# Kernel tuning notes

Measured on AMD Instinct MI355X. Metric: run time of the kernel, lower is better.

## Reference

```python
import jax, jax.numpy as jnp
import numpy as np
from jax import lax

ANG_RES = 9
MINDISP = -4
MAXDISP = 4
DN = ('NCHW', 'OIHW', 'NCHW')


def _dilat_pad(d, ang):
    if d < 0:
        dilat = abs(d) * ang + 1
        pad = (ang * (ang - 1) * abs(d)) // 2
    elif d == 0:
        dilat = 1
        pad = 0
    else:
        dilat = abs(d) * ang - 1
        pad = (ang * (ang - 1) * abs(d)) // 2 - ang + 1
    return dilat, pad


def setup_inputs() -> dict:
    key = jax.random.key(0)
    k1, k2 = jax.random.split(key)
    x = jax.random.normal(k1, (4, 64, 432, 432), dtype=jnp.float32)  # [B, Cin, angRes*H, angRes*W]
    W = jax.random.normal(k2, (64, 64, 9, 9), dtype=jnp.float32) * 0.05  # [Cout, Cin, angRes, angRes]
    return {"x": x, "W": W}


def reference(x, W):
    costs = []
    for d in range(MINDISP, MAXDISP + 1):
        dilat, pad = _dilat_pad(d, ANG_RES)
        cost = lax.conv_general_dilated(
            x, W,
            window_strides=(ANG_RES, ANG_RES),
            padding=[(pad, pad), (pad, pad)],
            rhs_dilation=(dilat, dilat),
            dimension_numbers=DN,
        )  # [B, Cout, H, W]
        costs.append(cost)
    # stack along new disparity axis -> [B, Cout, D, H, W]
    return jnp.stack(costs, axis=2)
```

## Files before the change

kernel.cpp:

```cpp
#include <hip/hip_runtime.h>

#define ANG 9
#define OHW 48
#define IMG 432
#define CIN 64
#define COUT 64
#define ND 9
#define NB 4
#define NVIEW 81
#define NSPAT 2304
#define NTOT 9216

#define SLABW 81
#define SLABSZ (80 * SLABW)

using f32x4 = __attribute__((ext_vector_type(4))) float;
using s16x8 = __attribute__((ext_vector_type(8))) short;

__device__ __forceinline__ unsigned short f2bf(float f) {
    unsigned u = __float_as_uint(f);
    unsigned r = (u + 0x7FFFu + ((u >> 16) & 1u)) >> 16;
    return (unsigned short)r;
}

__global__ void k_wpack(const float* __restrict__ w, unsigned short* __restrict__ aw) {
    int idx = blockIdx.x * 256 + threadIdx.x;
    if (idx >= NVIEW * 128 * 64) return;
    int ci = idx & 63;
    int m  = (idx >> 6) & 127;
    int uv = idx >> 13;
    int u = uv / 9, v = uv % 9;
    int co = m & 63, var = m >> 6;
    int uu = var ? 8 - u : u;
    int vv = var ? 8 - v : v;
    aw[idx] = f2bf(w[((size_t)(co * 64 + ci) * 9 + uu) * 9 + vv]);
}

__global__ __launch_bounds__(512, 4)
void k_fused(const float* __restrict__ x,
             const unsigned short* __restrict__ aw,
             unsigned short* __restrict__ y) {
    __shared__ unsigned short lx[IMG * 64];
    const int h = blockIdx.x, u = blockIdx.y, b = blockIdx.z;
    const int t = threadIdx.x;
    const int ih = 9 * h + u;
    const int lane = t & 63, wave = t >> 6;
    const int lr = lane & 15;
    const int lh = lane >> 4;
    const int mh = wave >> 2;
    const int mf = wave & 3;

    const unsigned short* abase =
        aw + (((size_t)(u * 9) * 128) + mh * 64 + mf * 16 + lr) * 64 + lh * 8;
    s16x8 a0[9];
#pragma unroll
    for (int v = 0; v < 9; ++v)
        a0[v] = *reinterpret_cast<const s16x8*>(abase + (size_t)v * 128 * 64);

    {
        const int tx = t & 127, ty = t >> 7;
        if (tx < 108) {
            const float* base = x + (((size_t)b * 64) * IMG + ih) * IMG + 4 * tx;
#pragma unroll 4
            for (int k = 0; k < 16; ++k) {
                const int ci = ty * 16 + k;
                const float4 v4 = *reinterpret_cast<const float4*>(
                    base + (size_t)ci * (IMG * IMG));
                unsigned short us[4] = {f2bf(v4.x), f2bf(v4.y), f2bf(v4.z), f2bf(v4.w)};
#pragma unroll
                for (int jj = 0; jj < 4; ++jj) {
                    const int iw = 4 * tx + jj;
                    const int sc = ci ^ (((iw >> 2) & 7) << 3);
                    lx[iw * 64 + sc] = us[jj];
                }
            }
        }
    }
    __syncthreads();

    const int m    = mh * 64 + mf * 16 + lr;
    const int n0g  = b * NSPAT + h * 48;

    s16x8 a1n = *reinterpret_cast<const s16x8*>(abase + 32);
#pragma unroll
    for (int v = 0; v < 9; ++v) {
        const int uv = u * 9 + v;
        const s16x8 a1 = a1n;
        if (v < 8)
            a1n = *reinterpret_cast<const s16x8*>(abase + (size_t)(v + 1) * 128 * 64 + 32);
#pragma unroll
        for (int nt = 0; nt < 3; ++nt) {
            const int iw = 9 * (nt * 16 + lr) + v;
            const int g  = (iw >> 2) & 7;
            const s16x8 b0 = *reinterpret_cast<const s16x8*>(&lx[iw * 64 + ((lh ^ g) * 8)]);
            const s16x8 b1 = *reinterpret_cast<const s16x8*>(&lx[iw * 64 + (((4 + lh) ^ g) * 8)]);

            f32x4 acc = (f32x4){0.f, 0.f, 0.f, 0.f};
            acc = __builtin_amdgcn_mfma_f32_16x16x32_bf16(b0, a0[v], acc, 0, 0, 0);
            acc = __builtin_amdgcn_mfma_f32_16x16x32_bf16(b1, a1,    acc, 0, 0, 0);

            const unsigned long long pk =
                  (unsigned long long)f2bf(acc[0])
                | ((unsigned long long)f2bf(acc[1]) << 16)
                | ((unsigned long long)f2bf(acc[2]) << 32)
                | ((unsigned long long)f2bf(acc[3]) << 48);
            *reinterpret_cast<unsigned long long*>(
                &y[((size_t)uv * 128 + m) * NTOT + n0g + nt * 16 + 4 * lh]) = pk;
        }
    }
}

__global__ __launch_bounds__(576)
void k_gather4(const unsigned short* __restrict__ y, float* __restrict__ out) {
    __shared__ float lds[2 * SLABSZ];
    const int co = blockIdx.x, b = blockIdx.y;
    const int tid = threadIdx.x;

    for (int i = tid; i < 2 * SLABSZ; i += 576) lds[i] = 0.f;

    const int var  = tid / 288;
    const int e0   = (tid % 288) * 8;
    const int srow = e0 / 48, scol = e0 % 48;
    const int ldst = var * SLABSZ + (16 + srow) * SLABW + 16 + scol;
    const unsigned short* ybase =
        y + ((size_t)(var * 64 + co)) * NTOT + (size_t)b * NSPAT + e0;

    const int hh = tid / 12;
    const int w0 = (tid % 12) * 4;
    const int center = (16 + hh) * SLABW + 16 + w0;

    float acc[9][4];
#pragma unroll
    for (int dd = 0; dd < 9; ++dd)
#pragma unroll
        for (int i = 0; i < 4; ++i) acc[dd][i] = 0.f;

    uint4 pre0 = *reinterpret_cast<const uint4*>(ybase);
    uint4 pre1 = *reinterpret_cast<const uint4*>(ybase + (size_t)128 * NTOT);
    __syncthreads();

    for (int uv = 0; uv < NVIEW; ++uv) {
        float4 lo, hi;
        lo.x = __uint_as_float(pre0.x << 16);
        lo.y = __uint_as_float(pre0.x & 0xffff0000u);
        lo.z = __uint_as_float(pre0.y << 16);
        lo.w = __uint_as_float(pre0.y & 0xffff0000u);
        hi.x = __uint_as_float(pre0.z << 16);
        hi.y = __uint_as_float(pre0.z & 0xffff0000u);
        hi.z = __uint_as_float(pre0.w << 16);
        hi.w = __uint_as_float(pre0.w & 0xffff0000u);
        *reinterpret_cast<float4*>(&lds[ldst])     = lo;
        *reinterpret_cast<float4*>(&lds[ldst + 4]) = hi;

        pre0 = pre1;
        if (uv + 2 < NVIEW)
            pre1 = *reinterpret_cast<const uint4*>(ybase + (size_t)(uv + 2) * 128 * NTOT);

        __syncthreads();

        const int uq = uv / 9, vq = uv % 9;
        const int step = (uq - 4) * SLABW + (vq - 4);
        int base = center + 4 * step;
#pragma unroll
        for (int dd = 0; dd < 9; ++dd) {
            const float* p = &lds[base + (dd > 4 ? SLABSZ : 0)];
            acc[dd][0] += p[0];
            acc[dd][1] += p[1];
            acc[dd][2] += p[2];
            acc[dd][3] += p[3];
            base -= step;
        }
        __syncthreads();
    }

    const size_t ob = (size_t)(b * 64 + co) * 9 * NSPAT + tid * 4;
#pragma unroll
    for (int dd = 0; dd < 9; ++dd) {
        float4 o;
        o.x = acc[dd][0]; o.y = acc[dd][1]; o.z = acc[dd][2]; o.w = acc[dd][3];
        *reinterpret_cast<float4*>(&out[ob + (size_t)dd * NSPAT]) = o;
    }
}

__global__ __launch_bounds__(192)
void cost_volume_direct(const float* __restrict__ x,
                        const float* __restrict__ w,
                        float* __restrict__ out) {
    const int ow      = threadIdx.x;
    const int oh      = blockIdx.y * 4 + threadIdx.y;
    const int co_tile = blockIdx.x & 7;
    const int dd      = blockIdx.x >> 3;
    const int b       = blockIdx.z;
    const int d       = dd - 4;
    const int co0     = co_tile * 8;

    int dilat, pad;
    if (d < 0)       { dilat = (-d) * ANG + 1; pad = 36 * (-d); }
    else if (d == 0) { dilat = 1;              pad = 0; }
    else             { dilat = d * ANG - 1;    pad = 36 * d - (ANG - 1); }

    const int ih0 = oh * ANG - pad;
    const int iw0 = ow * ANG - pad;

    float acc[8];
#pragma unroll
    for (int i = 0; i < 8; ++i) acc[i] = 0.f;

    const float* xb = x + (size_t)b * CIN * IMG * IMG;
    for (int kh = 0; kh < ANG; ++kh) {
        const int ih = ih0 + kh * dilat;
        if ((unsigned)ih >= (unsigned)IMG) continue;
        const float* xrow_base = xb + (size_t)ih * IMG;
        const float* wrow      = w + kh * ANG;
        for (int ci = 0; ci < CIN; ++ci) {
            const float* xrow = xrow_base + (size_t)ci * (IMG * IMG);
            float xv[ANG];
#pragma unroll
            for (int kw = 0; kw < ANG; ++kw) {
                const int iw  = iw0 + kw * dilat;
                const bool ok = ((unsigned)iw < (unsigned)IMG);
                const float vv = xrow[ok ? iw : 0];
                xv[kw] = ok ? vv : 0.f;
            }
            const float* wc = wrow + ci * (ANG * ANG);
#pragma unroll
            for (int i = 0; i < 8; ++i) {
                const float* wi = wc + (size_t)(co0 + i) * (CIN * ANG * ANG);
#pragma unroll
                for (int kw = 0; kw < ANG; ++kw)
                    acc[i] = fmaf(xv[kw], wi[kw], acc[i]);
            }
        }
    }
#pragma unroll
    for (int i = 0; i < 8; ++i) {
        const size_t o = ((((size_t)b * COUT + (co0 + i)) * ND + dd) * OHW + oh) * OHW + ow;
        out[o] = acc[i];
    }
}

extern "C" void kernel_launch(void* const* d_in, const int* in_sizes, int n_in,
                              void* d_out, int out_size, void* d_ws, size_t ws_size,
                              hipStream_t stream) {
    const float* x   = (const float*)d_in[0];
    const float* w   = (const float*)d_in[1];
    float*       out = (float*)d_out;

    const size_t AW_BYTES = (size_t)NVIEW * 128 * 64 * 2;
    const size_t Y_BYTES  = (size_t)NVIEW * 128 * NTOT * 2;
    const size_t NEED     = AW_BYTES + Y_BYTES;

    if (ws_size >= NEED) {
        unsigned short* aw = (unsigned short*)d_ws;
        unsigned short* yb = (unsigned short*)((char*)d_ws + AW_BYTES);

        k_wpack  <<<dim3((NVIEW * 128 * 64 + 255) / 256), dim3(256), 0, stream>>>(w, aw);
        k_fused  <<<dim3(OHW, ANG, NB), dim3(512), 0, stream>>>(x, aw, yb);
        k_gather4<<<dim3(COUT, NB), dim3(576), 0, stream>>>(yb, out);
    } else {
        dim3 grid(8 * ND, OHW / 4, NB);
        dim3 block(OHW, 4, 1);
        cost_volume_direct<<<grid, block, 0, stream>>>(x, w, out);
    }
}
```

Measured before the change: 227.4 us.

## Process batch in two halves to shrink intermediate buffer for cache residency

After: 320.1 us. 40.8% more time.

```diff
diff --git a/kernel.cpp b/kernel.cpp
--- a/kernel.cpp
+++ b/kernel.cpp
@@ -9,7 +9,7 @@
 #define NB 4
 #define NVIEW 81
 #define NSPAT 2304
-#define NTOT 9216
+#define NTOTP 4608
 
 #define SLABW 81
 #define SLABSZ (80 * SLABW)
@@ -39,9 +39,10 @@
 __global__ __launch_bounds__(512, 4)
 void k_fused(const float* __restrict__ x,
              const unsigned short* __restrict__ aw,
-             unsigned short* __restrict__ y) {
+             unsigned short* __restrict__ y, int pair) {
     __shared__ unsigned short lx[IMG * 64];
-    const int h = blockIdx.x, u = blockIdx.y, b = blockIdx.z;
+    const int h = blockIdx.x, u = blockIdx.y, bl = blockIdx.z;
+    const int b = pair * 2 + bl;
     const int t = threadIdx.x;
     const int ih = 9 * h + u;
     const int lane = t & 63, wave = t >> 6;
@@ -78,8 +79,8 @@
     }
     __syncthreads();
 
-    const int m    = mh * 64 + mf * 16 + lr;
-    const int n0g  = b * NSPAT + h * 48;
+    const int m   = mh * 64 + mf * 16 + lr;
+    const int n0g = bl * NSPAT + h * 48;
 
     s16x8 a1n = *reinterpret_cast<const s16x8*>(abase + 32);
 #pragma unroll
@@ -105,15 +106,17 @@
                 | ((unsigned long long)f2bf(acc[2]) << 32)
                 | ((unsigned long long)f2bf(acc[3]) << 48);
             *reinterpret_cast<unsigned long long*>(
-                &y[((size_t)uv * 128 + m) * NTOT + n0g + nt * 16 + 4 * lh]) = pk;
+                &y[((size_t)uv * 128 + m) * NTOTP + n0g + nt * 16 + 4 * lh]) = pk;
         }
     }
 }
 
 __global__ __launch_bounds__(576)
-void k_gather4(const unsigned short* __restrict__ y, float* __restrict__ out) {
+void k_gather4(const unsigned short* __restrict__ y, float* __restrict__ out,
+               int pair) {
     __shared__ float lds[2 * SLABSZ];
-    const int co = blockIdx.x, b = blockIdx.y;
+    const int co = blockIdx.x, bl = blockIdx.y;
+    const int b = pair * 2 + bl;
     const int tid = threadIdx.x;
 
     for (int i = tid; i < 2 * SLABSZ; i += 576) lds[i] = 0.f;
@@ -123,7 +126,7 @@
     const int srow = e0 / 48, scol = e0 % 48;
     const int ldst = var * SLABSZ + (16 + srow) * SLABW + 16 + scol;
     const unsigned short* ybase =
-        y + ((size_t)(var * 64 + co)) * NTOT + (size_t)b * NSPAT + e0;
+        y + ((size_t)(var * 64 + co)) * NTOTP + (size_t)bl * NSPAT + e0;
 
     const int hh = tid / 12;
     const int w0 = (tid % 12) * 4;
@@ -136,7 +139,7 @@
         for (int i = 0; i < 4; ++i) acc[dd][i] = 0.f;
 
     uint4 pre0 = *reinterpret_cast<const uint4*>(ybase);
-    uint4 pre1 = *reinterpret_cast<const uint4*>(ybase + (size_t)128 * NTOT);
+    uint4 pre1 = *reinterpret_cast<const uint4*>(ybase + (size_t)128 * NTOTP);
     __syncthreads();
 
     for (int uv = 0; uv < NVIEW; ++uv) {
@@ -154,7 +157,7 @@
 
         pre0 = pre1;
         if (uv + 2 < NVIEW)
-            pre1 = *reinterpret_cast<const uint4*>(ybase + (size_t)(uv + 2) * 128 * NTOT);
+            pre1 = *reinterpret_cast<const uint4*>(ybase + (size_t)(uv + 2) * 128 * NTOTP);
 
         __syncthreads();
 
@@ -247,16 +250,18 @@
     float*       out = (float*)d_out;
 
     const size_t AW_BYTES = (size_t)NVIEW * 128 * 64 * 2;
-    const size_t Y_BYTES  = (size_t)NVIEW * 128 * NTOT * 2;
+    const size_t Y_BYTES  = (size_t)NVIEW * 128 * NTOTP * 2;
     const size_t NEED     = AW_BYTES + Y_BYTES;
 
     if (ws_size >= NEED) {
         unsigned short* aw = (unsigned short*)d_ws;
         unsigned short* yb = (unsigned short*)((char*)d_ws + AW_BYTES);
 
-        k_wpack  <<<dim3((NVIEW * 128 * 64 + 255) / 256), dim3(256), 0, stream>>>(w, aw);
-        k_fused  <<<dim3(OHW, ANG, NB), dim3(512), 0, stream>>>(x, aw, yb);
-        k_gather4<<<dim3(COUT, NB), dim3(576), 0, stream>>>(yb, out);
+        k_wpack<<<dim3((NVIEW * 128 * 64 + 255) / 256), dim3(256), 0, stream>>>(w, aw);
+        for (int pair = 0; pair < 2; ++pair) {
+            k_fused  <<<dim3(OHW, ANG, 2), dim3(512), 0, stream>>>(x, aw, yb, pair);
+            k_gather4<<<dim3(COUT, 2),     dim3(576), 0, stream>>>(yb, out, pair);
+        }
     } else {
         dim3 grid(8 * ND, OHW / 4, NB);
         dim3 block(OHW, 4, 1);
```

## Process two output rows per block with register-prefetched second row

Applied to the files above, without the earlier changes.

Measured after the change: 286.9 us. +26.2%, slower.

```diff
diff --git a/kernel.cpp b/kernel.cpp
--- a/kernel.cpp
+++ b/kernel.cpp
@@ -36,58 +36,66 @@
     aw[idx] = f2bf(w[((size_t)(co * 64 + ci) * 9 + uu) * 9 + vv]);
 }
 
-__global__ __launch_bounds__(512, 4)
-void k_fused(const float* __restrict__ x,
-             const unsigned short* __restrict__ aw,
-             unsigned short* __restrict__ y) {
-    __shared__ unsigned short lx[IMG * 64];
-    const int h = blockIdx.x, u = blockIdx.y, b = blockIdx.z;
-    const int t = threadIdx.x;
-    const int ih = 9 * h + u;
-    const int lane = t & 63, wave = t >> 6;
-    const int lr = lane & 15;
-    const int lh = lane >> 4;
-    const int mh = wave >> 2;
-    const int mf = wave & 3;
-
-    const unsigned short* abase =
-        aw + (((size_t)(u * 9) * 128) + mh * 64 + mf * 16 + lr) * 64 + lh * 8;
-    s16x8 a0[9];
-#pragma unroll
-    for (int v = 0; v < 9; ++v)
-        a0[v] = *reinterpret_cast<const s16x8*>(abase + (size_t)v * 128 * 64);
-
-    {
-        const int tx = t & 127, ty = t >> 7;
-        if (tx < 108) {
-            const float* base = x + (((size_t)b * 64) * IMG + ih) * IMG + 4 * tx;
+__device__ __forceinline__ void stage_lds(unsigned short* lx,
+                                          const float* __restrict__ xrow, int t) {
+    const int tx = t & 127, ty = t >> 7;
+    if (tx < 108) {
+        const float* base = xrow + 4 * tx;
 #pragma unroll 4
-            for (int k = 0; k < 16; ++k) {
-                const int ci = ty * 16 + k;
-                const float4 v4 = *reinterpret_cast<const float4*>(
-                    base + (size_t)ci * (IMG * IMG));
-                unsigned short us[4] = {f2bf(v4.x), f2bf(v4.y), f2bf(v4.z), f2bf(v4.w)};
-#pragma unroll
-                for (int jj = 0; jj < 4; ++jj) {
-                    const int iw = 4 * tx + jj;
-                    const int sc = ci ^ (((iw >> 2) & 7) << 3);
-                    lx[iw * 64 + sc] = us[jj];
-                }
+        for (int k = 0; k < 16; ++k) {
+            const int ci = ty * 16 + k;
+            const float4 v4 = *reinterpret_cast<const float4*>(
+                base + (size_t)ci * (IMG * IMG));
+            unsigned short us[4] = {f2bf(v4.x), f2bf(v4.y), f2bf(v4.z), f2bf(v4.w)};
+#pragma unroll
+            for (int jj = 0; jj < 4; ++jj) {
+                const int iw = 4 * tx + jj;
+                const int sc = ci ^ (((iw >> 2) & 7) << 3);
+                lx[iw * 64 + sc] = us[jj];
             }
         }
     }
-    __syncthreads();
-
-    const int m    = mh * 64 + mf * 16 + lr;
-    const int n0g  = b * NSPAT + h * 48;
-
-    s16x8 a1n = *reinterpret_cast<const s16x8*>(abase + 32);
+}
+
+__device__ __forceinline__ void load_regs(float4 f[16],
+                                          const float* __restrict__ xrow, int t) {
+    const int tx = t & 127, ty = t >> 7;
+    if (tx < 108) {
+        const float* base = xrow + 4 * tx;
+#pragma unroll
+        for (int k = 0; k < 16; ++k)
+            f[k] = *reinterpret_cast<const float4*>(
+                base + (size_t)(ty * 16 + k) * (IMG * IMG));
+    }
+}
+
+__device__ __forceinline__ void write_regs(unsigned short* lx, const float4 f[16],
+                                           int t) {
+    const int tx = t & 127, ty = t >> 7;
+    if (tx < 108) {
+#pragma unroll
+        for (int k = 0; k < 16; ++k) {
+            const int ci = ty * 16 + k;
+            unsigned short us[4] = {f2bf(f[k].x), f2bf(f[k].y), f2bf(f[k].z), f2bf(f[k].w)};
+#pragma unroll
+            for (int jj = 0; jj < 4; ++jj) {
+                const int iw = 4 * tx + jj;
+                const int sc = ci ^ (((iw >> 2) & 7) << 3);
+                lx[iw * 64 + sc] = us[jj];
+            }
+        }
+    }
+}
+
+__device__ __forceinline__ void compute_store(const unsigned short* lx,
+                                              const unsigned short* __restrict__ abase,
+                                              unsigned short* __restrict__ y,
+                                              int u, int n0g, int m, int lr, int lh) {
 #pragma unroll
     for (int v = 0; v < 9; ++v) {
         const int uv = u * 9 + v;
-        const s16x8 a1 = a1n;
-        if (v < 8)
-            a1n = *reinterpret_cast<const s16x8*>(abase + (size_t)(v + 1) * 128 * 64 + 32);
+        const s16x8 a0 = *reinterpret_cast<const s16x8*>(abase + (size_t)v * 128 * 64);
+        const s16x8 a1 = *reinterpret_cast<const s16x8*>(abase + (size_t)v * 128 * 64 + 32);
 #pragma unroll
         for (int nt = 0; nt < 3; ++nt) {
             const int iw = 9 * (nt * 16 + lr) + v;
@@ -96,8 +104,8 @@
             const s16x8 b1 = *reinterpret_cast<const s16x8*>(&lx[iw * 64 + (((4 + lh) ^ g) * 8)]);
 
             f32x4 acc = (f32x4){0.f, 0.f, 0.f, 0.f};
-            acc = __builtin_amdgcn_mfma_f32_16x16x32_bf16(b0, a0[v], acc, 0, 0, 0);
-            acc = __builtin_amdgcn_mfma_f32_16x16x32_bf16(b1, a1,    acc, 0, 0, 0);
+            acc = __builtin_amdgcn_mfma_f32_16x16x32_bf16(b0, a0, acc, 0, 0, 0);
+            acc = __builtin_amdgcn_mfma_f32_16x16x32_bf16(b1, a1, acc, 0, 0, 0);
 
             const unsigned long long pk =
                   (unsigned long long)f2bf(acc[0])
@@ -108,6 +116,43 @@
                 &y[((size_t)uv * 128 + m) * NTOT + n0g + nt * 16 + 4 * lh]) = pk;
         }
     }
+}
+
+__global__ __launch_bounds__(512, 4)
+void k_fused(const float* __restrict__ x,
+             const unsigned short* __restrict__ aw,
+             unsigned short* __restrict__ y) {
+    __shared__ unsigned short lx[IMG * 64];
+    const int L = blockIdx.x;
+    const int logical = (L >> 3) + (L & 7) * 108;
+    const int hp = logical % 24;
+    const int u  = (logical / 24) % 9;
+    const int b  = logical / 216;
+    const int h0 = 2 * hp, h1 = 2 * hp + 1;
+    const int t = threadIdx.x;
+    const int lane = t & 63, wave = t >> 6;
+    const int lr = lane & 15;
+    const int lh = lane >> 4;
+    const int mh = wave >> 2;
+    const int mf = wave & 3;
+    const int m  = mh * 64 + mf * 16 + lr;
+
+    const unsigned short* abase =
+        aw + (((size_t)(u * 9) * 128) + mh * 64 + mf * 16 + lr) * 64 + lh * 8;
+    const float* xplane = x + ((size_t)b * 64) * (IMG * IMG);
+
+    stage_lds(lx, xplane + (size_t)(9 * h0 + u) * IMG, t);
+    __syncthreads();
+
+    float4 f[16];
+    load_regs(f, xplane + (size_t)(9 * h1 + u) * IMG, t);
+
+    compute_store(lx, abase, y, u, b * NSPAT + h0 * 48, m, lr, lh);
+    __syncthreads();
+
+    write_regs(lx, f, t);
+    __syncthreads();
+    compute_store(lx, abase, y, u, b * NSPAT + h1 * 48, m, lr, lh);
 }
 
 __global__ __launch_bounds__(576)
@@ -255,7 +300,7 @@
         unsigned short* yb = (unsigned short*)((char*)d_ws + AW_BYTES);
 
         k_wpack  <<<dim3((NVIEW * 128 * 64 + 255) / 256), dim3(256), 0, stream>>>(w, aw);
-        k_fused  <<<dim3(OHW, ANG, NB), dim3(512), 0, stream>>>(x, aw, yb);
+        k_fused  <<<dim3((OHW / 2) * ANG * NB), dim3(512), 0, stream>>>(x, aw, yb);
         k_gather4<<<dim3(COUT, NB), dim3(576), 0, stream>>>(yb, out);
     } else {
         dim3 grid(8 * ND, OHW / 4, NB);
```
